# Optimization experiments

Hardware: AMD Instinct MI355X
Metric: run time of the kernel (lower is better)

## Reference

```python
import jax, jax.numpy as jnp
import numpy as np

PRED_WEIGHT = 1.0
GT_WEIGHT = 1.0
EPS = 1e-9
P = 16384
G = 16384


def setup_inputs() -> dict:
    key = jax.random.key(0)
    k1, k2, k3, k4 = jax.random.split(key, 4)
    return {
        "pred_points": jax.random.normal(k1, (P, 3), dtype=jnp.float32),
        "gt_points": jax.random.normal(k2, (G, 3), dtype=jnp.float32),
        "w_pred": jax.random.uniform(k3, (P,), dtype=jnp.float32),
        "w_gt": jax.random.uniform(k4, (G,), dtype=jnp.float32),
    }


def reference(pred_points, gt_points, w_pred, w_gt):
    # squared pairwise distances: ||p||^2 + ||g||^2 - 2 p.g, clamped at 0
    p2 = jnp.sum(pred_points * pred_points, axis=1)  # (P,)
    g2 = jnp.sum(gt_points * gt_points, axis=1)      # (G,)
    d2 = p2[:, None] + g2[None, :] - 2.0 * (pred_points @ gt_points.T)  # (P, G)
    d2 = jnp.maximum(d2, 0.0)
    min_pred = jnp.min(d2, axis=1)  # (P,)
    min_gt = jnp.min(d2, axis=0)    # (G,)
    weighted_pred = jnp.sum(w_pred * min_pred) / jnp.maximum(jnp.sum(w_pred), EPS)
    weighted_gt = jnp.sum(w_gt * min_gt) / jnp.maximum(jnp.sum(w_gt), EPS)
    return PRED_WEIGHT * weighted_pred + GT_WEIGHT * weighted_gt
```

## Files before the change

kernel.cpp:

```cpp
#include <hip/hip_runtime.h>
#include <math.h>


constexpr int NPTS  = 16384;
constexpr int BLOCK = 512;
constexpr int WAVES = BLOCK / 64;

constexpr int ROWS_PER_BLOCK = 512;
constexpr int COLS_PER_BLOCK = 512;
constexpr int NBX = NPTS / ROWS_PER_BLOCK;
constexpr int NBY = NPTS / COLS_PER_BLOCK;
constexpr int NBLOCKS = NBX * NBY * 2;
constexpr int ROWS_PER_WAVE = ROWS_PER_BLOCK / WAVES;
constexpr int ATILES = ROWS_PER_WAVE / 32;
constexpr int CSTEPS = COLS_PER_BLOCK / 64;

typedef __attribute__((ext_vector_type(8)))  __bf16 bf16x8;
typedef __attribute__((ext_vector_type(16))) float  f32x16;

__device__ inline unsigned short f2bf(float f) {
    unsigned u = __float_as_uint(f);
    u += 0x7FFFu + ((u >> 16) & 1u);
    return (unsigned short)(u >> 16);
}
__device__ inline float bf2f(unsigned short h) {
    return __uint_as_float(((unsigned)h) << 16);
}
__device__ inline unsigned pk(unsigned short lo, unsigned short hi) {
    return (unsigned)lo | ((unsigned)hi << 16);
}

__global__ __launch_bounds__(256) void pack_init_kernel(
    const float* __restrict__ pred, const float* __restrict__ gt,
    uint4* __restrict__ Af, uint4* __restrict__ Bf,
    uint4* __restrict__ Ag, uint4* __restrict__ Bp,
    unsigned int* __restrict__ minP, unsigned int* __restrict__ minG,
    unsigned int* __restrict__ ticket)
{
    const unsigned short ONE = 0x3F80;
    int i = blockIdx.x * 256 + threadIdx.x;
    if (i == 0) *ticket = 0u;
    if (i >= NPTS) return;

    {
        float x = pred[3*i], y = pred[3*i+1], z = pred[3*i+2];
        unsigned short hx = f2bf(x), hy = f2bf(y), hz = f2bf(z);
        unsigned short lx = f2bf(x - bf2f(hx));
        unsigned short ly = f2bf(y - bf2f(hy));
        unsigned short lz = f2bf(z - bf2f(hz));
        float p2 = fmaf(x, x, fmaf(y, y, z * z));
        unsigned short sh = f2bf(p2), sl = f2bf(p2 - bf2f(sh));
        uint4 a0, a1, b0, b1;
        a0.x = pk(hx, hy); a0.y = pk(hz, lx); a0.z = pk(ly, lz); a0.w = pk(hx, hy);
        a1.x = pk(hz, sh); a1.y = pk(sl, ONE); a1.z = pk(ONE, lx); a1.w = pk(ly, lz);
        b0.x = pk(hx, hy); b0.y = pk(hz, hx); b0.z = pk(hy, hz); b0.w = pk(lx, ly);
        b1.x = pk(lz, ONE); b1.y = pk(ONE, sh); b1.z = pk(sl, lx); b1.w = pk(ly, lz);
        Af[i] = a0; Af[NPTS + i] = a1;
        Bp[i] = b0; Bp[NPTS + i] = b1;
    }
    {
        float gx = gt[3*i], gy = gt[3*i+1], gz = gt[3*i+2];
        float mx = -2.0f * gx, my = -2.0f * gy, mz = -2.0f * gz;
        unsigned short hx = f2bf(mx), hy = f2bf(my), hz = f2bf(mz);
        unsigned short lx = f2bf(mx - bf2f(hx));
        unsigned short ly = f2bf(my - bf2f(hy));
        unsigned short lz = f2bf(mz - bf2f(hz));
        float g2 = fmaf(gx, gx, fmaf(gy, gy, gz * gz));
        unsigned short sh = f2bf(g2), sl = f2bf(g2 - bf2f(sh));
        uint4 a0, a1, b0, b1;
        a0.x = pk(hx, hy); a0.y = pk(hz, lx); a0.z = pk(ly, lz); a0.w = pk(hx, hy);
        a1.x = pk(hz, sh); a1.y = pk(sl, ONE); a1.z = pk(ONE, lx); a1.w = pk(ly, lz);
        b0.x = pk(hx, hy); b0.y = pk(hz, hx); b0.z = pk(hy, hz); b0.w = pk(lx, ly);
        b1.x = pk(lz, ONE); b1.y = pk(ONE, sh); b1.z = pk(sl, lx); b1.w = pk(ly, lz);
        Ag[i] = a0; Ag[NPTS + i] = a1;
        Bf[i] = b0; Bf[NPTS + i] = b1;
    }
    minP[i] = 0x7F800000u;
    minG[i] = 0x7F800000u;
}

__device__ inline float tree16(const f32x16 a) {
    float m0 = fminf(fminf(a[0],  a[1]),  a[2]);
    float m1 = fminf(fminf(a[3],  a[4]),  a[5]);
    float m2 = fminf(fminf(a[6],  a[7]),  a[8]);
    float m3 = fminf(fminf(a[9],  a[10]), a[11]);
    float m4 = fminf(fminf(a[12], a[13]), a[14]);
    float m5 = fminf(fminf(m0, m1), m2);
    float m6 = fminf(fminf(m3, m4), a[15]);
    return fminf(m5, m6);
}

__global__ __launch_bounds__(BLOCK, 2) void chamfer_mfma_kernel(
    const uint4* __restrict__ Af, const uint4* __restrict__ Bf,
    const uint4* __restrict__ Ag, const uint4* __restrict__ Bp,
    unsigned int* __restrict__ minP, unsigned int* __restrict__ minG,
    const float* __restrict__ wpred, const float* __restrict__ wgt,
    unsigned int* __restrict__ ticket, float* __restrict__ out)
{
    const int tid  = threadIdx.x;
    const int wv   = tid >> 6;
    const int lane = tid & 63;
    const int half = lane >> 5;
    const int ln31 = lane & 31;

    const uint4* __restrict__ Aside;
    const uint4* __restrict__ Bside;
    unsigned int* __restrict__ outMin;
    if (blockIdx.z == 0) { Aside = Af; Bside = Bf; outMin = minG; }
    else                 { Aside = Ag; Bside = Bp; outMin = minP; }

    const int rowBase = blockIdx.x * ROWS_PER_BLOCK + wv * ROWS_PER_WAVE;
    const int colBase = blockIdx.y * COLS_PER_BLOCK;

    __shared__ uint4 sBf[2 * COLS_PER_BLOCK];
    __shared__ unsigned int cminS[COLS_PER_BLOCK];

    #pragma unroll
    for (int p = 0; p < (2 * COLS_PER_BLOCK) / BLOCK; ++p) {
        int idx = p * BLOCK + tid;
        int h = idx >> 9;
        int c = idx & (COLS_PER_BLOCK - 1);
        sBf[idx] = Bside[h * NPTS + colBase + c];
    }
    for (int c = tid; c < COLS_PER_BLOCK; c += BLOCK)
        cminS[c] = 0x7F800000u;
    __syncthreads();

    const uint4* __restrict__ Ah = Aside + half * NPTS;
    const uint4* sB = sBf + half * COLS_PER_BLOCK;

    const f32x16 zacc = {0.f,0.f,0.f,0.f, 0.f,0.f,0.f,0.f,
                         0.f,0.f,0.f,0.f, 0.f,0.f,0.f,0.f};

    #pragma unroll 1
    for (int a = 0; a < ATILES; ++a) {
        uint4 ac = Ah[rowBase + a * 32 + ln31];
        bf16x8 af = __builtin_bit_cast(bf16x8, ac);

        #pragma unroll 2
        for (int s = 0; s < CSTEPS; ++s) {
            bf16x8 b0 = __builtin_bit_cast(bf16x8, sB[s * 64 + ln31]);
            bf16x8 b1 = __builtin_bit_cast(bf16x8, sB[s * 64 + 32 + ln31]);
            f32x16 acc0 = __builtin_amdgcn_mfma_f32_32x32x16_bf16(af, b0, zacc, 0, 0, 0);
            f32x16 acc1 = __builtin_amdgcn_mfma_f32_32x32x16_bf16(af, b1, zacc, 0, 0, 0);
            float c0 = fmaxf(tree16(acc0), 0.0f);
            float c1 = fmaxf(tree16(acc1), 0.0f);
            c0 = fminf(c0, __shfl_xor(c0, 32, 64));
            c1 = fminf(c1, __shfl_xor(c1, 32, 64));
            if (half == 0) {
                atomicMin(&cminS[s * 64 + ln31],      __float_as_uint(c0));
                atomicMin(&cminS[s * 64 + 32 + ln31], __float_as_uint(c1));
            }
        }
    }

    __syncthreads();
    for (int c = tid; c < COLS_PER_BLOCK; c += BLOCK)
        atomicMin(&outMin[colBase + c], cminS[c]);

    __shared__ unsigned int sTicket;
    asm volatile("s_waitcnt vmcnt(0)" ::: "memory");
    __syncthreads();
    if (tid == 0) sTicket = atomicAdd(ticket, 1u);
    __syncthreads();
    if (sTicket != (unsigned)(NBLOCKS - 1)) return;

    float np = 0.f, dp = 0.f, ng = 0.f, dg = 0.f;
    for (int i = tid; i < NPTS; i += BLOCK) {
        float v = __uint_as_float(atomicMin(&minP[i], 0xFFFFFFFFu));
        float w = wpred[i];
        np = fmaf(w, v, np); dp += w;
        float u = __uint_as_float(atomicMin(&minG[i], 0xFFFFFFFFu));
        float x = wgt[i];
        ng = fmaf(x, u, ng); dg += x;
    }
    #pragma unroll
    for (int off = 1; off < 64; off <<= 1) {
        np += __shfl_xor(np, off, 64);
        dp += __shfl_xor(dp, off, 64);
        ng += __shfl_xor(ng, off, 64);
        dg += __shfl_xor(dg, off, 64);
    }
    __shared__ float sred[4][WAVES];
    if (lane == 0) { sred[0][wv] = np; sred[1][wv] = dp;
                     sred[2][wv] = ng; sred[3][wv] = dg; }
    __syncthreads();
    if (tid == 0) {
        float NP = 0.f, DP = 0.f, NG = 0.f, DG = 0.f;
        #pragma unroll
        for (int k = 0; k < WAVES; ++k) {
            NP += sred[0][k]; DP += sred[1][k];
            NG += sred[2][k]; DG += sred[3][k];
        }
        out[0] = NP / fmaxf(DP, 1e-9f) + NG / fmaxf(DG, 1e-9f);
    }
}

extern "C" void kernel_launch(void* const* d_in, const int* in_sizes, int n_in,
                              void* d_out, int out_size, void* d_ws, size_t ws_size,
                              hipStream_t stream)
{
    const float* pred  = (const float*)d_in[0];
    const float* gt    = (const float*)d_in[1];
    const float* wpred = (const float*)d_in[2];
    const float* wgt   = (const float*)d_in[3];
    float* out = (float*)d_out;

    uint4* Af = (uint4*)d_ws;
    uint4* Bf = Af + 2 * NPTS;
    uint4* Ag = Bf + 2 * NPTS;
    uint4* Bp = Ag + 2 * NPTS;
    unsigned int* minP = (unsigned int*)(Bp + 2 * NPTS);
    unsigned int* minG = minP + NPTS;
    unsigned int* ticket = minG + NPTS;

    pack_init_kernel<<<NPTS / 256, 256, 0, stream>>>(
        pred, gt, Af, Bf, Ag, Bp, minP, minG, ticket);

    chamfer_mfma_kernel<<<dim3(NBX, NBY, 2), BLOCK, 0, stream>>>(
        Af, Bf, Ag, Bp, minP, minG, wpred, wgt, ticket, out);
}
```

Before: 99.94 us.

## Give each block full rows for 64 columns, drop global atomics and ticket

Each block now owns 64 columns and scans all 16384 rows, with B fragments held in registers and a running min kept per lane. Inside the loop, LDS loads and per-step shared atomics are replaced by a single LDS reduction at the end. The global atomicMin arrays and the last-block ticket reduction are replaced by per-block weighted partial sums, which a small separate finalize kernel adds up. In exchange the grid shrinks to 512 blocks that each run a long serial loop, A is re-read from global/L2 by every block, and an extra kernel launch is added.

```diff
diff --git a/kernel.cpp b/kernel.cpp
--- a/kernel.cpp
+++ b/kernel.cpp
@@ -6,14 +6,10 @@
 constexpr int BLOCK = 512;
 constexpr int WAVES = BLOCK / 64;
 
-constexpr int ROWS_PER_BLOCK = 512;
-constexpr int COLS_PER_BLOCK = 512;
-constexpr int NBX = NPTS / ROWS_PER_BLOCK;
-constexpr int NBY = NPTS / COLS_PER_BLOCK;
-constexpr int NBLOCKS = NBX * NBY * 2;
-constexpr int ROWS_PER_WAVE = ROWS_PER_BLOCK / WAVES;
+constexpr int COLS_PER_BLOCK = 64;
+constexpr int NCB = NPTS / COLS_PER_BLOCK;
+constexpr int ROWS_PER_WAVE = NPTS / WAVES;
 constexpr int ATILES = ROWS_PER_WAVE / 32;
-constexpr int CSTEPS = COLS_PER_BLOCK / 64;
 
 typedef __attribute__((ext_vector_type(8)))  __bf16 bf16x8;
 typedef __attribute__((ext_vector_type(16))) float  f32x16;
@@ -33,13 +29,10 @@
 __global__ __launch_bounds__(256) void pack_init_kernel(
     const float* __restrict__ pred, const float* __restrict__ gt,
     uint4* __restrict__ Af, uint4* __restrict__ Bf,
-    uint4* __restrict__ Ag, uint4* __restrict__ Bp,
-    unsigned int* __restrict__ minP, unsigned int* __restrict__ minG,
-    unsigned int* __restrict__ ticket)
+    uint4* __restrict__ Ag, uint4* __restrict__ Bp)
 {
     const unsigned short ONE = 0x3F80;
     int i = blockIdx.x * 256 + threadIdx.x;
-    if (i == 0) *ticket = 0u;
     if (i >= NPTS) return;
 
     {
@@ -75,8 +68,6 @@
         Ag[i] = a0; Ag[NPTS + i] = a1;
         Bf[i] = b0; Bf[NPTS + i] = b1;
     }
-    minP[i] = 0x7F800000u;
-    minG[i] = 0x7F800000u;
 }
 
 __device__ inline float tree16(const f32x16 a) {
@@ -93,9 +84,8 @@
 __global__ __launch_bounds__(BLOCK, 2) void chamfer_mfma_kernel(
     const uint4* __restrict__ Af, const uint4* __restrict__ Bf,
     const uint4* __restrict__ Ag, const uint4* __restrict__ Bp,
-    unsigned int* __restrict__ minP, unsigned int* __restrict__ minG,
     const float* __restrict__ wpred, const float* __restrict__ wgt,
-    unsigned int* __restrict__ ticket, float* __restrict__ out)
+    float2* __restrict__ partials)
 {
     const int tid  = threadIdx.x;
     const int wv   = tid >> 6;
@@ -105,92 +95,86 @@
 
     const uint4* __restrict__ Aside;
     const uint4* __restrict__ Bside;
-    unsigned int* __restrict__ outMin;
-    if (blockIdx.z == 0) { Aside = Af; Bside = Bf; outMin = minG; }
-    else                 { Aside = Ag; Bside = Bp; outMin = minP; }
-
-    const int rowBase = blockIdx.x * ROWS_PER_BLOCK + wv * ROWS_PER_WAVE;
-    const int colBase = blockIdx.y * COLS_PER_BLOCK;
-
-    __shared__ uint4 sBf[2 * COLS_PER_BLOCK];
-    __shared__ unsigned int cminS[COLS_PER_BLOCK];
-
-    #pragma unroll
-    for (int p = 0; p < (2 * COLS_PER_BLOCK) / BLOCK; ++p) {
-        int idx = p * BLOCK + tid;
-        int h = idx >> 9;
-        int c = idx & (COLS_PER_BLOCK - 1);
-        sBf[idx] = Bside[h * NPTS + colBase + c];
-    }
-    for (int c = tid; c < COLS_PER_BLOCK; c += BLOCK)
-        cminS[c] = 0x7F800000u;
-    __syncthreads();
-
-    const uint4* __restrict__ Ah = Aside + half * NPTS;
-    const uint4* sB = sBf + half * COLS_PER_BLOCK;
+    const float* __restrict__ w;
+    if (blockIdx.y == 0) { Aside = Af; Bside = Bf; w = wgt;   }
+    else                 { Aside = Ag; Bside = Bp; w = wpred; }
+
+    const int colBase = blockIdx.x * COLS_PER_BLOCK;
+
+    bf16x8 bf0 = __builtin_bit_cast(bf16x8, Bside[half * NPTS + colBase + ln31]);
+    bf16x8 bf1 = __builtin_bit_cast(bf16x8, Bside[half * NPTS + colBase + 32 + ln31]);
+
+    const uint4* __restrict__ Ah = Aside + half * NPTS + wv * ROWS_PER_WAVE;
 
     const f32x16 zacc = {0.f,0.f,0.f,0.f, 0.f,0.f,0.f,0.f,
                          0.f,0.f,0.f,0.f, 0.f,0.f,0.f,0.f};
 
-    #pragma unroll 1
-    for (int a = 0; a < ATILES; ++a) {
-        uint4 ac = Ah[rowBase + a * 32 + ln31];
-        bf16x8 af = __builtin_bit_cast(bf16x8, ac);
-
-        #pragma unroll 2
-        for (int s = 0; s < CSTEPS; ++s) {
-            bf16x8 b0 = __builtin_bit_cast(bf16x8, sB[s * 64 + ln31]);
-            bf16x8 b1 = __builtin_bit_cast(bf16x8, sB[s * 64 + 32 + ln31]);
-            f32x16 acc0 = __builtin_amdgcn_mfma_f32_32x32x16_bf16(af, b0, zacc, 0, 0, 0);
-            f32x16 acc1 = __builtin_amdgcn_mfma_f32_32x32x16_bf16(af, b1, zacc, 0, 0, 0);
-            float c0 = fmaxf(tree16(acc0), 0.0f);
-            float c1 = fmaxf(tree16(acc1), 0.0f);
-            c0 = fminf(c0, __shfl_xor(c0, 32, 64));
-            c1 = fminf(c1, __shfl_xor(c1, 32, 64));
-            if (half == 0) {
-                atomicMin(&cminS[s * 64 + ln31],      __float_as_uint(c0));
-                atomicMin(&cminS[s * 64 + 32 + ln31], __float_as_uint(c1));
-            }
+    float rm0 = INFINITY, rm1 = INFINITY;
+
+    #pragma unroll 2
+    for (int t = 0; t < ATILES; ++t) {
+        bf16x8 af = __builtin_bit_cast(bf16x8, Ah[t * 32 + ln31]);
+        f32x16 a0 = __builtin_amdgcn_mfma_f32_32x32x16_bf16(af, bf0, zacc, 0, 0, 0);
+        f32x16 a1 = __builtin_amdgcn_mfma_f32_32x32x16_bf16(af, bf1, zacc, 0, 0, 0);
+        rm0 = fminf(rm0, tree16(a0));
+        rm1 = fminf(rm1, tree16(a1));
+    }
+
+    rm0 = fminf(rm0, __shfl_xor(rm0, 32, 64));
+    rm1 = fminf(rm1, __shfl_xor(rm1, 32, 64));
+
+    __shared__ unsigned int cmin[COLS_PER_BLOCK];
+    if (tid < COLS_PER_BLOCK) cmin[tid] = 0x7F800000u;
+    __syncthreads();
+    if (half == 0) {
+        atomicMin(&cmin[ln31],      __float_as_uint(fmaxf(rm0, 0.0f)));
+        atomicMin(&cmin[32 + ln31], __float_as_uint(fmaxf(rm1, 0.0f)));
+    }
+    __syncthreads();
+
+    if (tid < COLS_PER_BLOCK) {
+        float v  = __uint_as_float(cmin[tid]);
+        float wc = w[colBase + tid];
+        float num = wc * v;
+        float den = wc;
+        #pragma unroll
+        for (int off = 1; off < 64; off <<= 1) {
+            num += __shfl_xor(num, off, 64);
+            den += __shfl_xor(den, off, 64);
         }
-    }
-
-    __syncthreads();
-    for (int c = tid; c < COLS_PER_BLOCK; c += BLOCK)
-        atomicMin(&outMin[colBase + c], cminS[c]);
-
-    __shared__ unsigned int sTicket;
-    asm volatile("s_waitcnt vmcnt(0)" ::: "memory");
-    __syncthreads();
-    if (tid == 0) sTicket = atomicAdd(ticket, 1u);
-    __syncthreads();
-    if (sTicket != (unsigned)(NBLOCKS - 1)) return;
-
-    float np = 0.f, dp = 0.f, ng = 0.f, dg = 0.f;
-    for (int i = tid; i < NPTS; i += BLOCK) {
-        float v = __uint_as_float(atomicMin(&minP[i], 0xFFFFFFFFu));
-        float w = wpred[i];
-        np = fmaf(w, v, np); dp += w;
-        float u = __uint_as_float(atomicMin(&minG[i], 0xFFFFFFFFu));
-        float x = wgt[i];
-        ng = fmaf(x, u, ng); dg += x;
-    }
+        if (tid == 0)
+            partials[blockIdx.y * NCB + blockIdx.x] = make_float2(num, den);
+    }
+}
+
+__global__ __launch_bounds__(256) void finalize_kernel(
+    const float2* __restrict__ partials, float* __restrict__ out)
+{
+    const int tid  = threadIdx.x;
+    const int lane = tid & 63;
+    const int wv   = tid >> 6;
+
+    float2 p0 = partials[tid];
+    float2 p1 = partials[NCB + tid];
+    float ng = p0.x, dg = p0.y, np = p1.x, dp = p1.y;
+
     #pragma unroll
     for (int off = 1; off < 64; off <<= 1) {
+        ng += __shfl_xor(ng, off, 64);
+        dg += __shfl_xor(dg, off, 64);
         np += __shfl_xor(np, off, 64);
         dp += __shfl_xor(dp, off, 64);
-        ng += __shfl_xor(ng, off, 64);
-        dg += __shfl_xor(dg, off, 64);
-    }
-    __shared__ float sred[4][WAVES];
-    if (lane == 0) { sred[0][wv] = np; sred[1][wv] = dp;
-                     sred[2][wv] = ng; sred[3][wv] = dg; }
+    }
+    __shared__ float sred[4][4];
+    if (lane == 0) { sred[0][wv] = ng; sred[1][wv] = dg;
+                     sred[2][wv] = np; sred[3][wv] = dp; }
     __syncthreads();
     if (tid == 0) {
-        float NP = 0.f, DP = 0.f, NG = 0.f, DG = 0.f;
+        float NG = 0.f, DG = 0.f, NP = 0.f, DP = 0.f;
         #pragma unroll
-        for (int k = 0; k < WAVES; ++k) {
-            NP += sred[0][k]; DP += sred[1][k];
-            NG += sred[2][k]; DG += sred[3][k];
+        for (int k = 0; k < 4; ++k) {
+            NG += sred[0][k]; DG += sred[1][k];
+            NP += sred[2][k]; DP += sred[3][k];
         }
         out[0] = NP / fmaxf(DP, 1e-9f) + NG / fmaxf(DG, 1e-9f);
     }
@@ -210,13 +194,13 @@
     uint4* Bf = Af + 2 * NPTS;
     uint4* Ag = Bf + 2 * NPTS;
     uint4* Bp = Ag + 2 * NPTS;
-    unsigned int* minP = (unsigned int*)(Bp + 2 * NPTS);
-    unsigned int* minG = minP + NPTS;
-    unsigned int* ticket = minG + NPTS;
+    float2* partials = (float2*)(Bp + 2 * NPTS);
 
     pack_init_kernel<<<NPTS / 256, 256, 0, stream>>>(
-        pred, gt, Af, Bf, Ag, Bp, minP, minG, ticket);
-
-    chamfer_mfma_kernel<<<dim3(NBX, NBY, 2), BLOCK, 0, stream>>>(
-        Af, Bf, Ag, Bp, minP, minG, wpred, wgt, ticket, out);
-}
+        pred, gt, Af, Bf, Ag, Bp);
+
+    chamfer_mfma_kernel<<<dim3(NCB, 2), BLOCK, 0, stream>>>(
+        Af, Bf, Ag, Bp, wpred, wgt, partials);
+
+    finalize_kernel<<<1, 256, 0, stream>>>(partials, out);
+}
```

Result: faster. 84.48 us (-15.5%).
